# Performance work log

Measured on AMD Instinct MI355X. Metric: run time of the kernel, lower is better.

Reference implementation:

```python
import jax, jax.numpy as jnp
import numpy as np

N_NODES = 100000
N_EDGES = 1600000
N_FEAT = 32


def setup_inputs() -> dict:
    key = jax.random.key(0)
    k1, k2, k3, k4 = jax.random.split(key, 4)
    u = jax.random.normal(k1, (N_NODES, N_FEAT), dtype=jnp.float32)
    weights = jax.random.uniform(k2, (N_EDGES,), dtype=jnp.float32)
    row = jax.random.randint(k3, (N_EDGES,), 0, N_NODES)
    col = jax.random.randint(k4, (N_EDGES,), 0, N_NODES)
    edge_index = jnp.stack([row, col]).astype(jnp.int64)
    return {"u": u, "weights": weights, "edge_index": edge_index}


def reference(u, weights, edge_index):
    # row, col: [E]; u: [N, F]; weights: [E]
    row, col = edge_index[0], edge_index[1]
    diff = u[col] - u[row]                      # [E, F] edge gather + diff
    weighted_diff = weights[:, None] * diff     # [E, F]
    # scatter-add into node outputs (index_add_ on row)
    laplacian = jax.ops.segment_sum(weighted_diff, row, num_segments=u.shape[0])
    return laplacian
```

## Files before the change

kernel.cpp:

```cpp
#include <hip/hip_runtime.h>


#define NFEAT 32
#define BUCKET_BITS 7
#define HB 128
#define MAXNB 1024
#define CH 4096
#define HCAP 2560
#define KSTASH (HCAP / 512)
#define HBLK 64

typedef float nfloat4 __attribute__((ext_vector_type(4)));
typedef unsigned int nuint2 __attribute__((ext_vector_type(2)));

__device__ __forceinline__ float4 nt_load_f4(const float4* p) {
    nfloat4 v = __builtin_nontemporal_load((const nfloat4*)p);
    return make_float4(v.x, v.y, v.z, v.w);
}
__device__ __forceinline__ void nt_store_f4(float4* p, float4 v) {
    nfloat4 t = {v.x, v.y, v.z, v.w};
    __builtin_nontemporal_store(t, (nfloat4*)p);
}
__device__ __forceinline__ uint2 nt_load_u2(const uint2* p) {
    nuint2 v = __builtin_nontemporal_load((const nuint2*)p);
    uint2 r; r.x = v.x; r.y = v.y; return r;
}

__device__ __forceinline__ int wave_incl_scan(int v, int lane) {
#pragma unroll
    for (int off = 1; off < 64; off <<= 1) {
        int t = __shfl_up(v, off, 64);
        if (lane >= off) v += t;
    }
    return v;
}

__global__ __launch_bounds__(512) void hist_kernel(const int* __restrict__ row,
                                                   int* __restrict__ hist_part,
                                                   int* __restrict__ ticket,
                                                   int E) {
    __shared__ int h[MAXNB];
    int hb = blockIdx.x;
    if (hb == 0) {
        ticket[threadIdx.x] = 0;
        ticket[threadIdx.x + 512] = 0;
    }
    for (int i = threadIdx.x; i < MAXNB; i += 512) h[i] = 0;
    __syncthreads();
    int span = hb;
    int nspan = (E + 2047) >> 11;
    for (; span < nspan; span += HBLK) {
        int e = (span << 11) + threadIdx.x * 4;
        if (e + 3 < E) {
            int4 r4 = *(const int4*)(row + e);
            atomicAdd(&h[r4.x >> BUCKET_BITS], 1);
            atomicAdd(&h[r4.y >> BUCKET_BITS], 1);
            atomicAdd(&h[r4.z >> BUCKET_BITS], 1);
            atomicAdd(&h[r4.w >> BUCKET_BITS], 1);
        } else {
            for (int k = 0; k < 4; ++k)
                if (e + k < E)
                    atomicAdd(&h[row[e + k] >> BUCKET_BITS], 1);
        }
    }
    __syncthreads();
    int* dst = hist_part + (size_t)hb * MAXNB;
    for (int i = threadIdx.x; i < MAXNB; i += 512) dst[i] = h[i];
}

__global__ __launch_bounds__(512) void fill_conv_kernel(const int* __restrict__ row,
                                                        const int* __restrict__ col,
                                                        const float* __restrict__ w,
                                                        const int* __restrict__ hist_part,
                                                        int* __restrict__ ticket,
                                                        int* __restrict__ offsets,
                                                        uint2* __restrict__ csr,
                                                        const float4* __restrict__ u4,
                                                        ushort4* __restrict__ ub,
                                                        int n4, int E, int nChunks) {
    __shared__ int hist[MAXNB];
    __shared__ int delta[MAXNB];
    __shared__ uint2 so[CH];
    __shared__ unsigned short sbs[CH];

    if ((int)blockIdx.x >= nChunks) {
        int i = ((int)blockIdx.x - nChunks) * 512 + threadIdx.x;
        if (i < n4) {
            float4 v = nt_load_f4(&u4[i]);
            ushort4 o;
            unsigned x;
            x = __float_as_uint(v.x); x += 0x7fffu + ((x >> 16) & 1u); o.x = (unsigned short)(x >> 16);
            x = __float_as_uint(v.y); x += 0x7fffu + ((x >> 16) & 1u); o.y = (unsigned short)(x >> 16);
            x = __float_as_uint(v.z); x += 0x7fffu + ((x >> 16) & 1u); o.z = (unsigned short)(x >> 16);
            x = __float_as_uint(v.w); x += 0x7fffu + ((x >> 16) & 1u); o.w = (unsigned short)(x >> 16);
            ub[i] = o;
        }
        return;
    }

    int tid = threadIdx.x;
    int lane = tid & 63, wid = tid >> 6;
    int lo = blockIdx.x * CH;
    int n = min(E - lo, CH);
    bool full = (n == CH);
    int* wsum = (int*)so;

    hist[tid] = 0;
    hist[tid + 512] = 0;
    __syncthreads();

    int rst[CH / 512];
    if (full) {
#pragma unroll
        for (int k = 0; k < CH / 512; ++k) {
            int r = __builtin_nontemporal_load(&row[lo + tid + k * 512]);
            rst[k] = r;
            atomicAdd(&hist[r >> BUCKET_BITS], 1);
        }
    } else {
        for (int i = tid; i < n; i += 512)
            atomicAdd(&hist[__builtin_nontemporal_load(&row[lo + i]) >> BUCKET_BITS], 1);
    }

    int c0g = 0, c1g = 0;
    for (int p = 0; p < HBLK; ++p) {
        int2 v = ((const int2*)(hist_part + (size_t)p * MAXNB))[tid];
        c0g += v.x; c1g += v.y;
    }
    __syncthreads();

    int c0 = hist[2 * tid];
    int c1 = hist[2 * tid + 1];
    int pairL = c0 + c1;
    int pairG = c0g + c1g;
    int inclL = wave_incl_scan(pairL, lane);
    int inclG = wave_incl_scan(pairG, lane);
    if (lane == 63) { wsum[wid] = inclL; wsum[8 + wid] = inclG; }
    __syncthreads();
    int baseL = 0, baseG = 0;
#pragma unroll
    for (int i = 0; i < 8; ++i) {
        int vl = wsum[i], vg = wsum[8 + i];
        if (i < wid) { baseL += vl; baseG += vg; }
    }
    inclL += baseL;
    inclG += baseG;
    int exclL = inclL - pairL;
    int excl1 = exclL + c0;
    int gE0 = inclG - pairG;
    int gE1 = gE0 + c0g;

    if (blockIdx.x == 0) {
        offsets[2 * tid] = gE0;
        offsets[2 * tid + 1] = gE1;
        if (tid == 511) offsets[MAXNB] = inclG;
    }

    int g0 = gE0 + (c0 ? atomicAdd(&ticket[2 * tid], c0) : 0);
    int g1 = gE1 + (c1 ? atomicAdd(&ticket[2 * tid + 1], c1) : 0);
    hist[2 * tid] = exclL;
    hist[2 * tid + 1] = excl1;
    delta[2 * tid] = g0 - exclL;
    delta[2 * tid + 1] = g1 - excl1;
    __syncthreads();

    if (full) {
#pragma unroll
        for (int k = 0; k < CH / 512; ++k) {
            int i = tid + k * 512;
            int r = rst[k];
            unsigned c = (unsigned)__builtin_nontemporal_load(&col[lo + i]);
            float wt = __builtin_nontemporal_load(&w[lo + i]);
            int b = r >> BUCKET_BITS;
            uint2 p;
            p.x = ((unsigned)(r & (HB - 1)) << 25) | c;
            p.y = __float_as_uint(wt);
            int pos = atomicAdd(&hist[b], 1);
            so[pos] = p;
            sbs[pos] = (unsigned short)b;
        }
    } else {
        for (int i = tid; i < n; i += 512) {
            int r = __builtin_nontemporal_load(&row[lo + i]);
            unsigned c = (unsigned)__builtin_nontemporal_load(&col[lo + i]);
            float wt = __builtin_nontemporal_load(&w[lo + i]);
            int b = r >> BUCKET_BITS;
            uint2 p;
            p.x = ((unsigned)(r & (HB - 1)) << 25) | c;
            p.y = __float_as_uint(wt);
            int pos = atomicAdd(&hist[b], 1);
            so[pos] = p;
            sbs[pos] = (unsigned short)b;
        }
    }
    __syncthreads();

    for (int i = tid; i < n; i += 512) {
        csr[i + delta[sbs[i]]] = so[i];
    }
}

__global__ __launch_bounds__(512) void node_half_kernel(const ushort4* __restrict__ ub,
                                                        const float4* __restrict__ u4,
                                                        const int* __restrict__ offsets,
                                                        const uint2* __restrict__ csr,
                                                        float4* __restrict__ out4, int N) {
    __shared__ uint2 se[HCAP];
    __shared__ int hist[HB];
    __shared__ int starts[HB + 1];
    __shared__ int sc[HB];

    int b = blockIdx.x;
    int tid = threadIdx.x;
    int start = offsets[b];
    int end = offsets[b + 1];
    int cnt = end - start;

    if (tid < HB) hist[tid] = 0;
    __syncthreads();

    if (cnt <= HCAP) {
        uint2 rst[KSTASH];
#pragma unroll
        for (int k = 0; k < KSTASH; ++k) {
            int i = start + tid + k * 512;
            if (i < end) {
                uint2 p = nt_load_u2(&csr[i]);
                rst[k] = p;
                atomicAdd(&hist[p.x >> 25], 1);
            }
        }
        __syncthreads();
        int myc = (tid < HB) ? hist[tid] : 0;
        int lane = tid & 63;
        int incl = wave_incl_scan(myc, lane);
        if (lane == 63) sc[tid >> 6] = incl;
        __syncthreads();
        if (tid < HB) {
            if (tid >= 64) incl += sc[0];
            int excl = incl - myc;
            starts[tid] = excl;
            hist[tid] = excl;
            if (tid == HB - 1) starts[HB] = incl;
        }
        __syncthreads();
#pragma unroll
        for (int k = 0; k < KSTASH; ++k) {
            int i = start + tid + k * 512;
            if (i < end) {
                uint2 p = rst[k];
                int pos = atomicAdd(&hist[p.x >> 25], 1);
                se[pos] = p;
            }
        }
        __syncthreads();

        int wave = tid >> 6;
        int f4 = lane & 7;
        int s = lane >> 3;
        for (int g = wave; g < HB / 8; g += 8) {
            int node = g * 8 + s;
            int s0 = starts[node];
            int s1 = starts[node + 1];
            float4 acc0 = make_float4(0.f, 0.f, 0.f, 0.f);
            float4 acc1 = make_float4(0.f, 0.f, 0.f, 0.f);
            float4 acc2 = make_float4(0.f, 0.f, 0.f, 0.f);
            float4 acc3 = make_float4(0.f, 0.f, 0.f, 0.f);
            float ws0 = 0.f, ws1 = 0.f, ws2 = 0.f, ws3 = 0.f;
            int i = s0;
            for (; i + 3 < s1; i += 4) {
                uint2 pa = se[i];
                uint2 pb = se[i + 1];
                uint2 pc = se[i + 2];
                uint2 pd = se[i + 3];
                float wa = __uint_as_float(pa.y);
                float wb = __uint_as_float(pb.y);
                float wc = __uint_as_float(pc.y);
                float wd = __uint_as_float(pd.y);
                ushort4 ua = ub[(size_t)(pa.x & 0x01FFFFFFu) * 8 + f4];
                ushort4 ubv = ub[(size_t)(pb.x & 0x01FFFFFFu) * 8 + f4];
                ushort4 uc = ub[(size_t)(pc.x & 0x01FFFFFFu) * 8 + f4];
                ushort4 ud = ub[(size_t)(pd.x & 0x01FFFFFFu) * 8 + f4];
                acc0.x += wa * __uint_as_float((unsigned)ua.x << 16);
                acc0.y += wa * __uint_as_float((unsigned)ua.y << 16);
                acc0.z += wa * __uint_as_float((unsigned)ua.z << 16);
                acc0.w += wa * __uint_as_float((unsigned)ua.w << 16);
                ws0 += wa;
                acc1.x += wb * __uint_as_float((unsigned)ubv.x << 16);
                acc1.y += wb * __uint_as_float((unsigned)ubv.y << 16);
                acc1.z += wb * __uint_as_float((unsigned)ubv.z << 16);
                acc1.w += wb * __uint_as_float((unsigned)ubv.w << 16);
                ws1 += wb;
                acc2.x += wc * __uint_as_float((unsigned)uc.x << 16);
                acc2.y += wc * __uint_as_float((unsigned)uc.y << 16);
                acc2.z += wc * __uint_as_float((unsigned)uc.z << 16);
                acc2.w += wc * __uint_as_float((unsigned)uc.w << 16);
                ws2 += wc;
                acc3.x += wd * __uint_as_float((unsigned)ud.x << 16);
                acc3.y += wd * __uint_as_float((unsigned)ud.y << 16);
                acc3.z += wd * __uint_as_float((unsigned)ud.z << 16);
                acc3.w += wd * __uint_as_float((unsigned)ud.w << 16);
                ws3 += wd;
            }
            for (; i < s1; ++i) {
                uint2 p = se[i];
                float wt = __uint_as_float(p.y);
                ushort4 us = ub[(size_t)(p.x & 0x01FFFFFFu) * 8 + f4];
                acc0.x += wt * __uint_as_float((unsigned)us.x << 16);
                acc0.y += wt * __uint_as_float((unsigned)us.y << 16);
                acc0.z += wt * __uint_as_float((unsigned)us.z << 16);
                acc0.w += wt * __uint_as_float((unsigned)us.w << 16);
                ws0 += wt;
            }
            float4 acc;
            acc.x = (acc0.x + acc1.x) + (acc2.x + acc3.x);
            acc.y = (acc0.y + acc1.y) + (acc2.y + acc3.y);
            acc.z = (acc0.z + acc1.z) + (acc2.z + acc3.z);
            acc.w = (acc0.w + acc1.w) + (acc2.w + acc3.w);
            float ws_ = (ws0 + ws1) + (ws2 + ws3);
            int glob = b * HB + node;
            if (glob < N) {
                float4 ur = nt_load_f4(&u4[(size_t)glob * 8 + f4]);
                float4 o;
                o.x = acc.x - ws_ * ur.x;
                o.y = acc.y - ws_ * ur.y;
                o.z = acc.z - ws_ * ur.z;
                o.w = acc.w - ws_ * ur.w;
                nt_store_f4(&out4[(size_t)glob * 8 + f4], o);
            }
        }
    } else {
        float* tile = (float*)se;
        float* wsumf = (float*)sc;
        for (int i = tid; i < HB * NFEAT; i += 512) tile[i] = 0.f;
        if (tid < HB) wsumf[tid] = 0.f;
        __syncthreads();
        int f4 = tid & 7;
        for (int i = start + (tid >> 3); i < end; i += 64) {
            uint2 p = nt_load_u2(&csr[i]);
            int rl = (int)(p.x >> 25);
            int c = (int)(p.x & 0x01FFFFFFu);
            float wt = __uint_as_float(p.y);
            ushort4 us = ub[(size_t)c * 8 + f4];
            float* t = &tile[rl * NFEAT + f4 * 4];
            atomicAdd(t + 0, wt * __uint_as_float((unsigned)us.x << 16));
            atomicAdd(t + 1, wt * __uint_as_float((unsigned)us.y << 16));
            atomicAdd(t + 2, wt * __uint_as_float((unsigned)us.z << 16));
            atomicAdd(t + 3, wt * __uint_as_float((unsigned)us.w << 16));
            if (f4 == 0) atomicAdd(&wsumf[rl], wt);
        }
        __syncthreads();
#pragma unroll
        for (int pass = 0; pass < 2; ++pass) {
            int idx = pass * 512 + tid;
            int node = idx >> 3;
            int ff = idx & 7;
            int glob = b * HB + node;
            if (glob < N) {
                float4 ur = nt_load_f4(&u4[(size_t)glob * 8 + ff]);
                float ws_ = wsumf[node];
                const float* t = &tile[node * NFEAT + ff * 4];
                float4 o;
                o.x = t[0] - ws_ * ur.x;
                o.y = t[1] - ws_ * ur.y;
                o.z = t[2] - ws_ * ur.z;
                o.w = t[3] - ws_ * ur.w;
                nt_store_f4(&out4[(size_t)glob * 8 + ff], o);
            }
        }
    }
}


__global__ __launch_bounds__(256) void zero_out_kernel(float* __restrict__ out, int n) {
    int i = blockIdx.x * blockDim.x + threadIdx.x;
    if (i < n) out[i] = 0.0f;
}

__global__ __launch_bounds__(256) void scatter_lap_kernel(const float4* __restrict__ u4,
                                                          const float* __restrict__ w,
                                                          const int* __restrict__ row,
                                                          const int* __restrict__ col,
                                                          float* __restrict__ out, int n_edges) {
    int tid = blockIdx.x * blockDim.x + threadIdx.x;
    int e = tid >> 3;
    int f4 = tid & 7;
    if (e >= n_edges) return;
    int r = row[e];
    int c = col[e];
    float wt = w[e];
    float4 uc = u4[(size_t)c * 8 + f4];
    float4 ur = u4[(size_t)r * 8 + f4];
    float* o = out + (size_t)r * NFEAT + f4 * 4;
    atomicAdd(o + 0, wt * (uc.x - ur.x));
    atomicAdd(o + 1, wt * (uc.y - ur.y));
    atomicAdd(o + 2, wt * (uc.z - ur.z));
    atomicAdd(o + 3, wt * (uc.w - ur.w));
}

extern "C" void kernel_launch(void* const* d_in, const int* in_sizes, int n_in,
                              void* d_out, int out_size, void* d_ws, size_t ws_size,
                              hipStream_t stream) {
    const float* u = (const float*)d_in[0];
    const float* w = (const float*)d_in[1];
    const int* ei = (const int*)d_in[2];
    float* out = (float*)d_out;

    const int E = in_sizes[1];
    const int N = out_size / NFEAT;
    const int* row = ei;
    const int* col = ei + E;

    const int NBH = (N + HB - 1) >> BUCKET_BITS;

    const size_t histPartOff = 0;
    const size_t histPartBytes = ((size_t)HBLK * MAXNB * 4 + 255) & ~(size_t)255;
    const size_t offsetsOff = histPartOff + histPartBytes;
    const size_t offsetsBytes = ((size_t)(MAXNB + 1) * 4 + 255) & ~(size_t)255;
    const size_t ticketOff = offsetsOff + offsetsBytes;
    const size_t ticketBytes = ((size_t)MAXNB * 4 + 255) & ~(size_t)255;
    const size_t csrOff = ticketOff + ticketBytes;
    const size_t csrBytes = ((size_t)E * 8 + 255) & ~(size_t)255;
    const size_t ubOff = csrOff + csrBytes;
    const size_t ubBytes = ((size_t)N * NFEAT * 2 + 255) & ~(size_t)255;
    const size_t totalWs = ubOff + ubBytes;

    if (ws_size < totalWs || NBH > MAXNB - 1) {
        zero_out_kernel<<<(out_size + 255) / 256, 256, 0, stream>>>(out, out_size);
        long long threads_total = (long long)E * 8;
        scatter_lap_kernel<<<(unsigned)((threads_total + 255) / 256), 256, 0, stream>>>(
            (const float4*)u, w, row, col, out, E);
        return;
    }

    char* ws = (char*)d_ws;
    int* hist_part = (int*)(ws + histPartOff);
    int* offsets = (int*)(ws + offsetsOff);
    int* ticket = (int*)(ws + ticketOff);
    uint2* csr = (uint2*)(ws + csrOff);
    ushort4* ub = (ushort4*)(ws + ubOff);

    hist_kernel<<<HBLK, 512, 0, stream>>>(row, hist_part, ticket, E);

    int n4 = N * (NFEAT / 4);
    int convBlocks = (n4 + 511) / 512;
    const int nChunks = (E + CH - 1) / CH;
    fill_conv_kernel<<<nChunks + convBlocks, 512, 0, stream>>>(row, col, w, hist_part,
                                                               ticket, offsets, csr,
                                                               (const float4*)u, ub,
                                                               n4, E, nChunks);

    node_half_kernel<<<NBH, 512, 0, stream>>>(ub, (const float4*)u, offsets, csr,
                                              (float4*)out, N);
}
```

Before: 140.9 us.

## Fuse histogram pass into fill kernel using a global completion counter spin-wait

The separate histogram kernel is folded into the fill/convert kernel as its first HBLK blocks. Each histogram block publishes its partial counts and increments a done counter, and the chunk blocks spin on that counter before reading the partial histograms. A hipMemsetAsync replaces the launch to reset the counter. This removes one kernel launch boundary and lets the chunks' local histograms overlap the global histogram. In exchange it relies on co-residency of the spinning blocks, guarded by a chunk-count cap, and adds a memset node.

```diff
diff --git a/kernel.cpp b/kernel.cpp
--- a/kernel.cpp
+++ b/kernel.cpp
@@ -35,56 +35,54 @@
     return v;
 }
 
-__global__ __launch_bounds__(512) void hist_kernel(const int* __restrict__ row,
-                                                   int* __restrict__ hist_part,
-                                                   int* __restrict__ ticket,
-                                                   int E) {
-    __shared__ int h[MAXNB];
-    int hb = blockIdx.x;
-    if (hb == 0) {
-        ticket[threadIdx.x] = 0;
-        ticket[threadIdx.x + 512] = 0;
-    }
-    for (int i = threadIdx.x; i < MAXNB; i += 512) h[i] = 0;
-    __syncthreads();
-    int span = hb;
-    int nspan = (E + 2047) >> 11;
-    for (; span < nspan; span += HBLK) {
-        int e = (span << 11) + threadIdx.x * 4;
-        if (e + 3 < E) {
-            int4 r4 = *(const int4*)(row + e);
-            atomicAdd(&h[r4.x >> BUCKET_BITS], 1);
-            atomicAdd(&h[r4.y >> BUCKET_BITS], 1);
-            atomicAdd(&h[r4.z >> BUCKET_BITS], 1);
-            atomicAdd(&h[r4.w >> BUCKET_BITS], 1);
-        } else {
-            for (int k = 0; k < 4; ++k)
-                if (e + k < E)
-                    atomicAdd(&h[row[e + k] >> BUCKET_BITS], 1);
-        }
-    }
-    __syncthreads();
-    int* dst = hist_part + (size_t)hb * MAXNB;
-    for (int i = threadIdx.x; i < MAXNB; i += 512) dst[i] = h[i];
-}
-
-__global__ __launch_bounds__(512) void fill_conv_kernel(const int* __restrict__ row,
-                                                        const int* __restrict__ col,
-                                                        const float* __restrict__ w,
-                                                        const int* __restrict__ hist_part,
-                                                        int* __restrict__ ticket,
-                                                        int* __restrict__ offsets,
-                                                        uint2* __restrict__ csr,
-                                                        const float4* __restrict__ u4,
-                                                        ushort4* __restrict__ ub,
-                                                        int n4, int E, int nChunks) {
+__global__ __launch_bounds__(512) void hist_fill_conv_kernel(
+        const int* __restrict__ row, const int* __restrict__ col,
+        const float* __restrict__ w, int* __restrict__ hist_part,
+        int* __restrict__ ticket, int* __restrict__ done,
+        int* __restrict__ offsets, uint2* __restrict__ csr,
+        const float4* __restrict__ u4, ushort4* __restrict__ ub,
+        int n4, int E, int nChunks) {
     __shared__ int hist[MAXNB];
     __shared__ int delta[MAXNB];
     __shared__ uint2 so[CH];
     __shared__ unsigned short sbs[CH];
 
-    if ((int)blockIdx.x >= nChunks) {
-        int i = ((int)blockIdx.x - nChunks) * 512 + threadIdx.x;
+    int tid = threadIdx.x;
+    int bid = (int)blockIdx.x;
+
+    if (bid < HBLK) {
+        if (bid == 0) {
+            ticket[tid] = 0;
+            ticket[tid + 512] = 0;
+        }
+        for (int i = tid; i < MAXNB; i += 512) hist[i] = 0;
+        __syncthreads();
+        int nspan = (E + 2047) >> 11;
+        for (int span = bid; span < nspan; span += HBLK) {
+            int e = (span << 11) + tid * 4;
+            if (e + 3 < E) {
+                int4 r4 = *(const int4*)(row + e);
+                atomicAdd(&hist[r4.x >> BUCKET_BITS], 1);
+                atomicAdd(&hist[r4.y >> BUCKET_BITS], 1);
+                atomicAdd(&hist[r4.z >> BUCKET_BITS], 1);
+                atomicAdd(&hist[r4.w >> BUCKET_BITS], 1);
+            } else {
+                for (int k = 0; k < 4; ++k)
+                    if (e + k < E)
+                        atomicAdd(&hist[row[e + k] >> BUCKET_BITS], 1);
+            }
+        }
+        __syncthreads();
+        int* dst = hist_part + (size_t)bid * MAXNB;
+        for (int i = tid; i < MAXNB; i += 512) dst[i] = hist[i];
+        __threadfence();
+        __syncthreads();
+        if (tid == 0) atomicAdd(done, 1);
+        return;
+    }
+
+    if (bid >= HBLK + nChunks) {
+        int i = (bid - HBLK - nChunks) * 512 + tid;
         if (i < n4) {
             float4 v = nt_load_f4(&u4[i]);
             ushort4 o;
@@ -98,9 +96,9 @@
         return;
     }
 
-    int tid = threadIdx.x;
+    int cb = bid - HBLK;
     int lane = tid & 63, wid = tid >> 6;
-    int lo = blockIdx.x * CH;
+    int lo = cb * CH;
     int n = min(E - lo, CH);
     bool full = (n == CH);
     int* wsum = (int*)so;
@@ -121,6 +119,13 @@
         for (int i = tid; i < n; i += 512)
             atomicAdd(&hist[__builtin_nontemporal_load(&row[lo + i]) >> BUCKET_BITS], 1);
     }
+
+    if (tid == 0) {
+        while (__hip_atomic_load(done, __ATOMIC_ACQUIRE,
+                                 __HIP_MEMORY_SCOPE_AGENT) < HBLK) {}
+    }
+    __syncthreads();
+    __threadfence();
 
     int c0g = 0, c1g = 0;
     for (int p = 0; p < HBLK; ++p) {
@@ -150,7 +155,7 @@
     int gE0 = inclG - pairG;
     int gE1 = gE0 + c0g;
 
-    if (blockIdx.x == 0) {
+    if (cb == 0) {
         offsets[2 * tid] = gE0;
         offsets[2 * tid + 1] = gE1;
         if (tid == 511) offsets[MAXNB] = inclG;
@@ -412,6 +417,7 @@
     const int* col = ei + E;
 
     const int NBH = (N + HB - 1) >> BUCKET_BITS;
+    const int nChunks = (E + CH - 1) / CH;
 
     const size_t histPartOff = 0;
     const size_t histPartBytes = ((size_t)HBLK * MAXNB * 4 + 255) & ~(size_t)255;
@@ -419,13 +425,15 @@
     const size_t offsetsBytes = ((size_t)(MAXNB + 1) * 4 + 255) & ~(size_t)255;
     const size_t ticketOff = offsetsOff + offsetsBytes;
     const size_t ticketBytes = ((size_t)MAXNB * 4 + 255) & ~(size_t)255;
-    const size_t csrOff = ticketOff + ticketBytes;
+    const size_t doneOff = ticketOff + ticketBytes;
+    const size_t doneBytes = 256;
+    const size_t csrOff = doneOff + doneBytes;
     const size_t csrBytes = ((size_t)E * 8 + 255) & ~(size_t)255;
     const size_t ubOff = csrOff + csrBytes;
     const size_t ubBytes = ((size_t)N * NFEAT * 2 + 255) & ~(size_t)255;
     const size_t totalWs = ubOff + ubBytes;
 
-    if (ws_size < totalWs || NBH > MAXNB - 1) {
+    if (ws_size < totalWs || NBH > MAXNB - 1 || nChunks > 600) {
         zero_out_kernel<<<(out_size + 255) / 256, 256, 0, stream>>>(out, out_size);
         long long threads_total = (long long)E * 8;
         scatter_lap_kernel<<<(unsigned)((threads_total + 255) / 256), 256, 0, stream>>>(
@@ -437,18 +445,17 @@
     int* hist_part = (int*)(ws + histPartOff);
     int* offsets = (int*)(ws + offsetsOff);
     int* ticket = (int*)(ws + ticketOff);
+    int* done = (int*)(ws + doneOff);
     uint2* csr = (uint2*)(ws + csrOff);
     ushort4* ub = (ushort4*)(ws + ubOff);
 
-    hist_kernel<<<HBLK, 512, 0, stream>>>(row, hist_part, ticket, E);
+    hipMemsetAsync(done, 0, sizeof(int), stream);
 
     int n4 = N * (NFEAT / 4);
     int convBlocks = (n4 + 511) / 512;
-    const int nChunks = (E + CH - 1) / CH;
-    fill_conv_kernel<<<nChunks + convBlocks, 512, 0, stream>>>(row, col, w, hist_part,
-                                                               ticket, offsets, csr,
-                                                               (const float4*)u, ub,
-                                                               n4, E, nChunks);
+    hist_fill_conv_kernel<<<HBLK + nChunks + convBlocks, 512, 0, stream>>>(
+        row, col, w, hist_part, ticket, done, offsets, csr,
+        (const float4*)u, ub, n4, E, nChunks);
 
     node_half_kernel<<<NBH, 512, 0, stream>>>(ub, (const float4*)u, offsets, csr,
                                               (float4*)out, N);
```

Result: slower. 247.0 us (+75.3%).
